# Kernel optimization log

Hardware: AMD Instinct MI355X
Metric: run time of the kernel (lower is better)

The kernel has to match this reference:

```python
import jax, jax.numpy as jnp
import numpy as np
from jax.scipy.special import logsumexp

N_STATES = 512
VOCAB = 10000
BATCH = 64
T_MAX = 1024


def setup_inputs() -> dict:
    key = jax.random.key(0)
    k1, k2, k3, k4, k5 = jax.random.split(key, 5)
    x = jax.random.randint(k1, (BATCH, T_MAX), 0, VOCAB)
    T = jax.random.randint(k2, (BATCH,), 1, T_MAX + 1)  # lengths in [1, T_max]
    priors = jax.random.normal(k3, (N_STATES,), dtype=jnp.float32)
    trans = jax.random.normal(k4, (N_STATES, N_STATES), dtype=jnp.float32)
    emit = jax.random.normal(k5, (N_STATES, VOCAB), dtype=jnp.float32)
    return {"x": x, "T": T, "priors": priors, "trans": trans, "emit": emit}


def reference(x, T, priors, trans, emit):
    # x: (B, Tmax) int, T: (B,) int lengths
    log_pi = jax.nn.log_softmax(priors)            # (N,)
    log_T = jax.nn.log_softmax(trans, axis=0)      # (N, N), columns normalized (dim=0 in torch)
    log_E = jax.nn.log_softmax(emit, axis=1)       # (N, M)

    em = log_E.T[x]                                # (B, Tmax, N) emission log-probs per timestep
    la0 = em[:, 0] + log_pi                        # (B, N)

    def step(la_prev, em_t):
        # out[b, j] = logsumexp_k log_T[j, k] + la_prev[b, k]
        la_new = em_t + logsumexp(log_T[None, :, :] + la_prev[:, None, :], axis=2)
        return la_new, logsumexp(la_new, axis=1)   # carry, per-step log-sum over states

    _, sums = jax.lax.scan(step, la0, jnp.moveaxis(em[:, 1:], 1, 0))  # sums: (Tmax-1, B)
    log_sums = jnp.concatenate([logsumexp(la0, axis=1)[None, :], sums], axis=0)  # (Tmax, B)

    idx = jnp.clip(T, 1, x.shape[1]) - 1           # (B,)
    log_probs = jnp.take_along_axis(log_sums.T, idx[:, None], axis=1)  # (B, 1)
    return log_probs
```

## Files before the change

kernel.cpp:

```cpp
#include <hip/hip_runtime.h>
#include <hip/hip_bf16.h>


typedef unsigned long long u64;
typedef unsigned int u32;
typedef unsigned short u16;
using f32x4 = __attribute__((ext_vector_type(4))) float;
using i32x8 = __attribute__((ext_vector_type(8))) int;

#define N_ST 512
#define VOCAB 10000
#define BATCH 64
#define T_MAX 1024

#define WS_EB       0
#define WS_GB       10240000
#define WS_A8       20480000
#define WS_ROWLSE   20742144
#define WS_COLLSE   20744192
#define WS_PINORM   20746240

static __device__ __forceinline__ float bf16f(u16 h) {
    return __uint_as_float((u32)h << 16);
}
static __device__ __forceinline__ u16 bf16enc(float f) {
    u32 u = __float_as_uint(f);
    return (u16)((u + 0x7fffu + ((u >> 16) & 1u)) >> 16);
}

static __device__ __forceinline__ float dec8(u32 b) {
    float nrm = __uint_as_float((b << 20) + 0x3C000000u);
    float dnm = (float)b * 0x1p-9f;
    return b >= 8u ? nrm : dnm;
}

static __device__ __forceinline__ u32 enc_e4m3(float f) {
    if (!(f > 0.f)) return 0u;
    unsigned u = __float_as_uint(f);
    int e = (int)((u >> 23) & 0xff) - 127;
    unsigned m = u & 0x7fffffu;
    if (e > 8 || (e == 8 && m >= 0x700000u)) return 0x7eu;
    if (e >= -6) {
        unsigned mant = m >> 20;
        unsigned rest = m & 0xfffffu;
        if (rest > 0x80000u || (rest == 0x80000u && (mant & 1u))) mant++;
        unsigned r = ((unsigned)(e + 7) << 3) + mant;
        return r > 0x7eu ? 0x7eu : r;
    }
    if (e < -10) return 0u;
    unsigned full = 0x800000u | m;
    int shift = 23 - (e + 9);
    unsigned r = full >> shift;
    unsigned rem = full & ((1u << shift) - 1u);
    unsigned half = 1u << (shift - 1);
    if (rem > half || (rem == half && (r & 1u))) r++;
    return r;
}

template <bool HI>
static __device__ __forceinline__ u32 cvtpk2(float a, float b, u32 old) {
#if __has_builtin(__builtin_amdgcn_cvt_pk_fp8_f32)
    return (u32)__builtin_amdgcn_cvt_pk_fp8_f32(a, b, (int)old, HI);
#else
    unsigned v = enc_e4m3(a) | (enc_e4m3(b) << 8);
    return HI ? ((old & 0x0000ffffu) | (v << 16)) : ((old & 0xffff0000u) | v);
#endif
}

__global__ __launch_bounds__(256) void k_row_lse(const float* __restrict__ emit,
                                                 float* __restrict__ rowLSE) {
    const int n = blockIdx.x;
    const float* row = emit + (size_t)n * VOCAB;
    __shared__ float redm[4], reds[4];
    const int tid = threadIdx.x, lane = tid & 63, wid = tid >> 6;

    float m = -INFINITY;
    for (int i = tid; i < VOCAB; i += 256) m = fmaxf(m, row[i]);
    #pragma unroll
    for (int o = 32; o; o >>= 1) m = fmaxf(m, __shfl_down(m, o));
    if (lane == 0) redm[wid] = m;
    __syncthreads();
    if (tid == 0) redm[0] = fmaxf(fmaxf(redm[0], redm[1]), fmaxf(redm[2], redm[3]));
    __syncthreads();
    m = redm[0];

    float s = 0.f;
    for (int i = tid; i < VOCAB; i += 256) s += __expf(row[i] - m);
    #pragma unroll
    for (int o = 32; o; o >>= 1) s += __shfl_down(s, o);
    if (lane == 0) reds[wid] = s;
    __syncthreads();
    if (tid == 0) rowLSE[n] = m + __logf(reds[0] + reds[1] + reds[2] + reds[3]);
}

__global__ __launch_bounds__(256) void k_expEmitT(const float* __restrict__ emit,
                                                  const float* __restrict__ rowLSE,
                                                  u16* __restrict__ Eb) {
    const size_t gid = (size_t)blockIdx.x * 256 + threadIdx.x;
    const int m = (int)(gid >> 9);
    const int n = (int)(gid & 511);
    Eb[gid] = bf16enc(__expf(emit[(size_t)n * VOCAB + m] - rowLSE[n]));
}

__global__ __launch_bounds__(256) void k_col_lse(const float* __restrict__ trans,
                                                 float* __restrict__ colLSE) {
    const int k = blockIdx.x;
    const int tid = threadIdx.x, lane = tid & 63, wid = tid >> 6;
    __shared__ float redm[4], reds[4];

    float a = trans[(size_t)tid * N_ST + k];
    float b = trans[(size_t)(tid + 256) * N_ST + k];
    float m = fmaxf(a, b);
    #pragma unroll
    for (int o = 32; o; o >>= 1) m = fmaxf(m, __shfl_down(m, o));
    if (lane == 0) redm[wid] = m;
    __syncthreads();
    if (tid == 0) redm[0] = fmaxf(fmaxf(redm[0], redm[1]), fmaxf(redm[2], redm[3]));
    __syncthreads();
    m = redm[0];

    float s = __expf(a - m) + __expf(b - m);
    #pragma unroll
    for (int o = 32; o; o >>= 1) s += __shfl_down(s, o);
    if (lane == 0) reds[wid] = s;
    __syncthreads();
    if (tid == 0) colLSE[k] = m + __logf(reds[0] + reds[1] + reds[2] + reds[3]);
}

__global__ __launch_bounds__(64) void k_packA_fp8(const float* __restrict__ trans,
                                                  const float* __restrict__ colLSE,
                                                  u32* __restrict__ A8) {
    const int f = blockIdx.x;
    const int l = threadIdx.x;
    const int w = f >> 4, ks = (f >> 2) & 3, jt = f & 3;
    const int j = w * 64 + jt * 16 + (l & 15);
    const int k0 = ks * 128 + (l >> 4) * 32;
    u32 dw[8];
    #pragma unroll
    for (int d = 0; d < 8; ++d) {
        float a0 = 256.0f * __expf(trans[(size_t)j * N_ST + k0 + 4 * d + 0] - colLSE[k0 + 4 * d + 0]);
        float a1 = 256.0f * __expf(trans[(size_t)j * N_ST + k0 + 4 * d + 1] - colLSE[k0 + 4 * d + 1]);
        float a2 = 256.0f * __expf(trans[(size_t)j * N_ST + k0 + 4 * d + 2] - colLSE[k0 + 4 * d + 2]);
        float a3 = 256.0f * __expf(trans[(size_t)j * N_ST + k0 + 4 * d + 3] - colLSE[k0 + 4 * d + 3]);
        u32 pk = cvtpk2<false>(a0, a1, 0u);
        dw[d] = cvtpk2<true>(a2, a3, pk);
    }
    u32* dst = A8 + (size_t)f * 512 + l * 8;
    *(uint4*)dst       = make_uint4(dw[0], dw[1], dw[2], dw[3]);
    *(uint4*)(dst + 4) = make_uint4(dw[4], dw[5], dw[6], dw[7]);
}

__global__ __launch_bounds__(512) void k_pinorm(const float* __restrict__ priors,
                                                float* __restrict__ pinorm) {
    const int j = threadIdx.x, lane = j & 63, wid = j >> 6;
    __shared__ float redm[8], reds[8];
    float v = priors[j];

    float m = v;
    #pragma unroll
    for (int o = 32; o; o >>= 1) m = fmaxf(m, __shfl_down(m, o));
    if (lane == 0) redm[wid] = m;
    __syncthreads();
    if (j == 0) {
        float r = redm[0];
        for (int i = 1; i < 8; ++i) r = fmaxf(r, redm[i]);
        redm[0] = r;
    }
    __syncthreads();
    m = redm[0];

    float s = __expf(v - m);
    #pragma unroll
    for (int o = 32; o; o >>= 1) s += __shfl_down(s, o);
    if (lane == 0) reds[wid] = s;
    __syncthreads();
    if (j == 0) {
        float r = 0.f;
        for (int i = 0; i < 8; ++i) r += reds[i];
        reds[0] = r;
    }
    __syncthreads();
    pinorm[j] = __expf(v - m) / reds[0];
}

__global__ __launch_bounds__(256) void k_G(const u16* __restrict__ Eb,
                                           const float* __restrict__ trans,
                                           const float* __restrict__ colLSE,
                                           u16* __restrict__ Gb) {
    __shared__ float Es[16][512];
    const int m0 = blockIdx.x * 16;
    const int tid = threadIdx.x;
    for (int idx = tid; idx < 16 * 512; idx += 256)
        Es[idx >> 9][idx & 511] = bf16f(Eb[(size_t)(m0 + (idx >> 9)) * 512 + (idx & 511)]);
    __syncthreads();

    const int k0 = tid, k1 = tid + 256;
    const float c0 = colLSE[k0], c1 = colLSE[k1];
    float acc0[16], acc1[16];
    #pragma unroll
    for (int mi = 0; mi < 16; ++mi) { acc0[mi] = 0.f; acc1[mi] = 0.f; }

    for (int j = 0; j < 512; ++j) {
        float a0 = __expf(trans[(size_t)j * N_ST + k0] - c0);
        float a1 = __expf(trans[(size_t)j * N_ST + k1] - c1);
        #pragma unroll
        for (int mi = 0; mi < 16; ++mi) {
            float e = Es[mi][j];
            acc0[mi] = fmaf(e, a0, acc0[mi]);
            acc1[mi] = fmaf(e, a1, acc1[mi]);
        }
    }
    #pragma unroll
    for (int mi = 0; mi < 16; ++mi) {
        Gb[(size_t)(m0 + mi) * N_ST + k0] = bf16enc(acc0[mi]);
        Gb[(size_t)(m0 + mi) * N_ST + k1] = bf16enc(acc1[mi]);
    }
}

#define UNIT_SCALES 0x7f7f7f7f

#define STEP_BODY(EU, GU, EP, GP)                                               \
  {                                                                             \
    const int xpre = xnext;                                                     \
    GP = *(const uint4*)((const char*)Gb + ((size_t)xpre << 10) + (l << 4));    \
    _Pragma("unroll")                                                           \
    for (int jt = 0; jt < 4; ++jt)                                              \
      EP[jt] = *(const u64*)(Eb + (size_t)xpre * N_ST + wbase + jt * 16 + rbase); \
    xnext = xb[(t + 2 <= Tf) ? (t + 2) : Tf];                                   \
    const u64 vown = vq[p][l];                                                  \
    const u32* vbase = (const u32*)&vq[p][0];                                   \
    f32x4 ac0={0,0,0,0}, ac1={0,0,0,0}, ac2={0,0,0,0}, ac3={0,0,0,0};           \
    _Pragma("unroll")                                                           \
    for (int ks = 0; ks < 4; ++ks) {                                            \
      const uint4 b0 = *(const uint4*)(vbase + ks * 32 + grp * 8);              \
      const uint4 b1 = *(const uint4*)(vbase + ks * 32 + grp * 8 + 4);          \
      const i32x8 bq = {(int)b0.x, (int)b0.y, (int)b0.z, (int)b0.w,             \
                        (int)b1.x, (int)b1.y, (int)b1.z, (int)b1.w};            \
      ac0 = __builtin_amdgcn_mfma_scale_f32_16x16x128_f8f6f4(                   \
                af[ks * 4 + 0], bq, ac0, 0, 0, 0, UNIT_SCALES, 0, UNIT_SCALES); \
      ac1 = __builtin_amdgcn_mfma_scale_f32_16x16x128_f8f6f4(                   \
                af[ks * 4 + 1], bq, ac1, 0, 0, 0, UNIT_SCALES, 0, UNIT_SCALES); \
      ac2 = __builtin_amdgcn_mfma_scale_f32_16x16x128_f8f6f4(                   \
                af[ks * 4 + 2], bq, ac2, 0, 0, 0, UNIT_SCALES, 0, UNIT_SCALES); \
      ac3 = __builtin_amdgcn_mfma_scale_f32_16x16x128_f8f6f4(                   \
                af[ks * 4 + 3], bq, ac3, 0, 0, 0, UNIT_SCALES, 0, UNIT_SCALES); \
    }                                                                           \
    float gv = 0.f;                                                             \
    {                                                                           \
      const u32 gw[4] = {GU.x, GU.y, GU.z, GU.w};                               \
      _Pragma("unroll")                                                         \
      for (int i = 0; i < 4; ++i) {                                             \
        float g0 = bf16f((u16)(gw[i] & 0xffffu));                               \
        float g1 = bf16f((u16)(gw[i] >> 16));                                   \
        float v0 = dec8((u32)(vown >> (16 * i)) & 0xffu);                       \
        float v1 = dec8((u32)(vown >> (16 * i + 8)) & 0xffu);                   \
        gv = fmaf(g0, v0, gv);                                                  \
        gv = fmaf(g1, v1, gv);                                                  \
      }                                                                         \
      _Pragma("unroll")                                                         \
      for (int o = 1; o <= 32; o <<= 1) gv += __shfl_xor(gv, o);                \
    }                                                                           \
    float wv2[16];                                                              \
    _Pragma("unroll")                                                           \
    for (int r = 0; r < 4; ++r) {                                               \
      wv2[0 + r]  = bf16f((u16)(EU[0] >> (16 * r))) * ac0[r];                   \
      wv2[4 + r]  = bf16f((u16)(EU[1] >> (16 * r))) * ac1[r];                   \
      wv2[8 + r]  = bf16f((u16)(EU[2] >> (16 * r))) * ac2[r];                   \
      wv2[12 + r] = bf16f((u16)(EU[3] >> (16 * r))) * ac3[r];                   \
    }                                                                           \
    if (t == Tf) {                                                              \
      float s2 = 0.f;                                                           \
      _Pragma("unroll")                                                         \
      for (int i = 0; i < 16; ++i) s2 += wv2[i];                                \
      s2 += __shfl_xor(s2, 16);                                                 \
      s2 += __shfl_xor(s2, 32);                                                 \
      if (l == 0) red[wid] = s2;                                                \
      __syncthreads();                                                          \
      const float Se = red[0] + red[1] + red[2] + red[3] +                      \
                       red[4] + red[5] + red[6] + red[7];                       \
      if (tid == 0) out[b] = L + __logf(Se) - (float)Tb * LN256;                \
    } else {                                                                    \
      L += __logf(gv);                                                          \
      const float sc = 1.0f / gv;                                               \
      if ((l & 15) == 0) {                                                      \
        u32* vw = (u32*)&vq[p ^ 1][0];                                          \
        _Pragma("unroll")                                                       \
        for (int jt = 0; jt < 4; ++jt) {                                        \
          u32 pk = cvtpk2<false>(wv2[jt * 4 + 0] * sc, wv2[jt * 4 + 1] * sc, 0u); \
          pk = cvtpk2<true>(wv2[jt * 4 + 2] * sc, wv2[jt * 4 + 3] * sc, pk);    \
          vw[(wbase >> 2) + jt * 4 + grp] = pk;                                 \
        }                                                                       \
      }                                                                         \
      __syncthreads();                                                          \
      p ^= 1;                                                                   \
    }                                                                           \
  }

__global__ __launch_bounds__(512, 2) void hmm_main(const int* __restrict__ x,
                                                   const int* __restrict__ T,
                                                   const u16* __restrict__ Eb,
                                                   const u32* __restrict__ A8,
                                                   const u16* __restrict__ Gb,
                                                   const float* __restrict__ pinorm,
                                                   float* __restrict__ out) {
    __shared__ u64 vq[2][64];
    __shared__ float red[8];
    const int b = blockIdx.x;
    const int tid = threadIdx.x;
    const int l = tid & 63;
    const int wid = tid >> 6;
    const int grp = l >> 4;
    const int wbase = wid * 64;
    const int rbase = grp * 4;
    const float LN256 = 5.545177444479562f;

    int Tb = T[b];
    Tb = Tb < 1 ? 1 : (Tb > T_MAX ? T_MAX : Tb);
    const int* xb = x + (size_t)b * T_MAX;

    i32x8 af[16];
    {
        const u32* ap = A8 + (size_t)wid * 16 * 512 + l * 8;
        #pragma unroll
        for (int i = 0; i < 16; ++i) {
            uint4 lo = *(const uint4*)(ap + (size_t)i * 512);
            uint4 hi = *(const uint4*)(ap + (size_t)i * 512 + 4);
            af[i] = i32x8{(int)lo.x, (int)lo.y, (int)lo.z, (int)lo.w,
                          (int)hi.x, (int)hi.y, (int)hi.z, (int)hi.w};
        }
    }

    const int x0 = xb[0];
    const int x1 = xb[1];
    u64 eA[4], eB[4];
    uint4 gA, gB;
    gA = *(const uint4*)((const char*)Gb + ((size_t)x1 << 10) + (l << 4));
    #pragma unroll
    for (int jt = 0; jt < 4; ++jt)
        eA[jt] = *(const u64*)(Eb + (size_t)x1 * N_ST + wbase + jt * 16 + rbase);

    float wv[16];
    float s = 0.f;
    #pragma unroll
    for (int jt = 0; jt < 4; ++jt) {
        u64 eraw = *(const u64*)(Eb + (size_t)x0 * N_ST + wbase + jt * 16 + rbase);
        #pragma unroll
        for (int r = 0; r < 4; ++r) {
            const int j = wbase + jt * 16 + rbase + r;
            float e = bf16f((u16)(eraw >> (16 * r)));
            float t0 = e * pinorm[j];
            wv[jt * 4 + r] = t0;
            s += t0;
        }
    }
    s += __shfl_xor(s, 16);
    s += __shfl_xor(s, 32);
    if (l == 0) red[wid] = s;
    __syncthreads();
    float S0 = red[0] + red[1] + red[2] + red[3] + red[4] + red[5] + red[6] + red[7];
    float L = __logf(S0);
    if (Tb == 1) {
        if (tid == 0) out[b] = L;
        return;
    }
    __syncthreads();
    {
        const float sc = 256.0f / S0;
        if ((l & 15) == 0) {
            u32* vw = (u32*)&vq[0][0];
            #pragma unroll
            for (int jt = 0; jt < 4; ++jt) {
                u32 pk = cvtpk2<false>(wv[jt * 4 + 0] * sc, wv[jt * 4 + 1] * sc, 0u);
                pk = cvtpk2<true>(wv[jt * 4 + 2] * sc, wv[jt * 4 + 3] * sc, pk);
                vw[(wbase >> 2) + jt * 4 + grp] = pk;
            }
        }
    }
    __syncthreads();

    const int Tf = Tb - 1;
    int p = 0;
    int xnext = xb[(2 <= Tf) ? 2 : Tf];
    for (int t = 1;;) {
        STEP_BODY(eA, gA, eB, gB)
        if (t == Tf) break;
        ++t;
        STEP_BODY(eB, gB, eA, gA)
        if (t == Tf) break;
        ++t;
    }
}

extern "C" void kernel_launch(void* const* d_in, const int* in_sizes, int n_in,
                              void* d_out, int out_size, void* d_ws, size_t ws_size,
                              hipStream_t stream) {
    const int*   x      = (const int*)d_in[0];
    const int*   T      = (const int*)d_in[1];
    const float* priors = (const float*)d_in[2];
    const float* trans  = (const float*)d_in[3];
    const float* emit   = (const float*)d_in[4];
    float* out = (float*)d_out;

    char* ws = (char*)d_ws;
    u16*   Eb     = (u16*)(ws + WS_EB);
    u16*   Gb     = (u16*)(ws + WS_GB);
    u32*   A8     = (u32*)(ws + WS_A8);
    float* rowLSE = (float*)(ws + WS_ROWLSE);
    float* colLSE = (float*)(ws + WS_COLLSE);
    float* pinorm = (float*)(ws + WS_PINORM);

    k_row_lse<<<N_ST, 256, 0, stream>>>(emit, rowLSE);
    k_expEmitT<<<(VOCAB * N_ST) / 256, 256, 0, stream>>>(emit, rowLSE, Eb);
    k_col_lse<<<N_ST, 256, 0, stream>>>(trans, colLSE);
    k_packA_fp8<<<128, 64, 0, stream>>>(trans, colLSE, A8);
    k_pinorm<<<1, 512, 0, stream>>>(priors, pinorm);
    k_G<<<VOCAB / 16, 256, 0, stream>>>(Eb, trans, colLSE, Gb);

    hmm_main<<<BATCH, 512, 0, stream>>>(x, T, Eb, A8, Gb, pinorm, out);
}
```

Measured before the change: 1.332 ms.

## Quantize transition matrix to block-scaled FP4 with per-row E8M0 scales

Replaces the FP8 packing of the exponentiated transition matrix with FP4 (E2M1) values plus a per-32-element E8M0 block scale, and feeds them to the scaled MFMA with the A operand format set to FP4 and the scale selected per opsel. This halves the register footprint of the resident A fragments (16 x uint4 instead of 16 x i32x8), which could ease register pressure and raise occupancy, and may reduce MFMA cost. The price is a much coarser quantization of transition probabilities, which risks accuracy loss, and the scale packing and indexing are intricate.

```diff
diff --git a/kernel.cpp b/kernel.cpp
--- a/kernel.cpp
+++ b/kernel.cpp
@@ -15,10 +15,11 @@
 
 #define WS_EB       0
 #define WS_GB       10240000
-#define WS_A8       20480000
-#define WS_ROWLSE   20742144
-#define WS_COLLSE   20744192
-#define WS_PINORM   20746240
+#define WS_A4       20480000
+#define WS_ASC      20611072
+#define WS_ROWLSE   20643840
+#define WS_COLLSE   20645888
+#define WS_PINORM   20647936
 
 static __device__ __forceinline__ float bf16f(u16 h) {
     return __uint_as_float((u32)h << 16);
@@ -127,27 +128,38 @@
     if (tid == 0) colLSE[k] = m + __logf(reds[0] + reds[1] + reds[2] + reds[3]);
 }
 
-__global__ __launch_bounds__(64) void k_packA_fp8(const float* __restrict__ trans,
+__global__ __launch_bounds__(64) void k_packA_fp4(const float* __restrict__ trans,
                                                   const float* __restrict__ colLSE,
-                                                  u32* __restrict__ A8) {
+                                                  u32* __restrict__ A4,
+                                                  unsigned char* __restrict__ ASC) {
     const int f = blockIdx.x;
     const int l = threadIdx.x;
     const int w = f >> 4, ks = (f >> 2) & 3, jt = f & 3;
     const int j = w * 64 + jt * 16 + (l & 15);
     const int k0 = ks * 128 + (l >> 4) * 32;
-    u32 dw[8];
-    #pragma unroll
-    for (int d = 0; d < 8; ++d) {
-        float a0 = 256.0f * __expf(trans[(size_t)j * N_ST + k0 + 4 * d + 0] - colLSE[k0 + 4 * d + 0]);
-        float a1 = 256.0f * __expf(trans[(size_t)j * N_ST + k0 + 4 * d + 1] - colLSE[k0 + 4 * d + 1]);
-        float a2 = 256.0f * __expf(trans[(size_t)j * N_ST + k0 + 4 * d + 2] - colLSE[k0 + 4 * d + 2]);
-        float a3 = 256.0f * __expf(trans[(size_t)j * N_ST + k0 + 4 * d + 3] - colLSE[k0 + 4 * d + 3]);
-        u32 pk = cvtpk2<false>(a0, a1, 0u);
-        dw[d] = cvtpk2<true>(a2, a3, pk);
-    }
-    u32* dst = A8 + (size_t)f * 512 + l * 8;
-    *(uint4*)dst       = make_uint4(dw[0], dw[1], dw[2], dw[3]);
-    *(uint4*)(dst + 4) = make_uint4(dw[4], dw[5], dw[6], dw[7]);
+
+    float e[32];
+    float m = 0.f;
+    #pragma unroll
+    for (int k = 0; k < 32; ++k) {
+        e[k] = 256.0f * __expf(trans[(size_t)j * N_ST + k0 + k] - colLSE[k0 + k]);
+        m = fmaxf(m, e[k]);
+    }
+    const int eexp = (int)ceilf(log2f(m * (1.0f / 6.0f)));
+    const float inv = exp2f((float)(-eexp));
+
+    u32 dw[4] = {0u, 0u, 0u, 0u};
+    #pragma unroll
+    for (int k = 0; k < 32; ++k) {
+        const float xv = e[k] * inv;
+        u32 q = xv < 0.25f ? 0u : xv < 0.75f ? 1u : xv < 1.25f ? 2u :
+                xv < 1.75f ? 3u : xv < 2.5f  ? 4u : xv < 3.5f  ? 5u :
+                xv < 5.0f  ? 6u : 7u;
+        dw[k >> 3] |= q << (4 * (k & 7));
+    }
+    u32* dst = A4 + (size_t)f * 256 + l * 4;
+    *(uint4*)dst = make_uint4(dw[0], dw[1], dw[2], dw[3]);
+    ASC[(size_t)(((w * 4 + ks) * 64 + l) * 4) + jt] = (unsigned char)(127 + eexp);
 }
 
 __global__ __launch_bounds__(512) void k_pinorm(const float* __restrict__ priors,
@@ -218,6 +230,7 @@
 }
 
 #define UNIT_SCALES 0x7f7f7f7f
+#define AFRAG(i) (i32x8{(int)af[i].x, (int)af[i].y, (int)af[i].z, (int)af[i].w, 0, 0, 0, 0})
 
 #define STEP_BODY(EU, GU, EP, GP)                                               \
   {                                                                             \
@@ -237,13 +250,13 @@
       const i32x8 bq = {(int)b0.x, (int)b0.y, (int)b0.z, (int)b0.w,             \
                         (int)b1.x, (int)b1.y, (int)b1.z, (int)b1.w};            \
       ac0 = __builtin_amdgcn_mfma_scale_f32_16x16x128_f8f6f4(                   \
-                af[ks * 4 + 0], bq, ac0, 0, 0, 0, UNIT_SCALES, 0, UNIT_SCALES); \
+                AFRAG(ks * 4 + 0), bq, ac0, 4, 0, 0, (int)asc[ks], 0, UNIT_SCALES); \
       ac1 = __builtin_amdgcn_mfma_scale_f32_16x16x128_f8f6f4(                   \
-                af[ks * 4 + 1], bq, ac1, 0, 0, 0, UNIT_SCALES, 0, UNIT_SCALES); \
+                AFRAG(ks * 4 + 1), bq, ac1, 4, 0, 1, (int)asc[ks], 0, UNIT_SCALES); \
       ac2 = __builtin_amdgcn_mfma_scale_f32_16x16x128_f8f6f4(                   \
-                af[ks * 4 + 2], bq, ac2, 0, 0, 0, UNIT_SCALES, 0, UNIT_SCALES); \
+                AFRAG(ks * 4 + 2), bq, ac2, 4, 0, 2, (int)asc[ks], 0, UNIT_SCALES); \
       ac3 = __builtin_amdgcn_mfma_scale_f32_16x16x128_f8f6f4(                   \
-                af[ks * 4 + 3], bq, ac3, 0, 0, 0, UNIT_SCALES, 0, UNIT_SCALES); \
+                AFRAG(ks * 4 + 3), bq, ac3, 4, 0, 3, (int)asc[ks], 0, UNIT_SCALES); \
     }                                                                           \
     float gv = 0.f;                                                             \
     {                                                                           \
@@ -299,7 +312,8 @@
 __global__ __launch_bounds__(512, 2) void hmm_main(const int* __restrict__ x,
                                                    const int* __restrict__ T,
                                                    const u16* __restrict__ Eb,
-                                                   const u32* __restrict__ A8,
+                                                   const u32* __restrict__ A4,
+                                                   const u32* __restrict__ ASC,
                                                    const u16* __restrict__ Gb,
                                                    const float* __restrict__ pinorm,
                                                    float* __restrict__ out) {
@@ -318,16 +332,16 @@
     Tb = Tb < 1 ? 1 : (Tb > T_MAX ? T_MAX : Tb);
     const int* xb = x + (size_t)b * T_MAX;
 
-    i32x8 af[16];
+    uint4 af[16];
+    u32 asc[4];
     {
-        const u32* ap = A8 + (size_t)wid * 16 * 512 + l * 8;
+        const u32* ap = A4 + (size_t)wid * 16 * 256 + l * 4;
         #pragma unroll
-        for (int i = 0; i < 16; ++i) {
-            uint4 lo = *(const uint4*)(ap + (size_t)i * 512);
-            uint4 hi = *(const uint4*)(ap + (size_t)i * 512 + 4);
-            af[i] = i32x8{(int)lo.x, (int)lo.y, (int)lo.z, (int)lo.w,
-                          (int)hi.x, (int)hi.y, (int)hi.z, (int)hi.w};
-        }
+        for (int i = 0; i < 16; ++i)
+            af[i] = *(const uint4*)(ap + (size_t)i * 256);
+        #pragma unroll
+        for (int d = 0; d < 4; ++d)
+            asc[d] = ASC[(wid * 4 + d) * 64 + l];
     }
 
     const int x0 = xb[0];
@@ -404,7 +418,8 @@
     char* ws = (char*)d_ws;
     u16*   Eb     = (u16*)(ws + WS_EB);
     u16*   Gb     = (u16*)(ws + WS_GB);
-    u32*   A8     = (u32*)(ws + WS_A8);
+    u32*   A4     = (u32*)(ws + WS_A4);
+    unsigned char* ASCb = (unsigned char*)(ws + WS_ASC);
     float* rowLSE = (float*)(ws + WS_ROWLSE);
     float* colLSE = (float*)(ws + WS_COLLSE);
     float* pinorm = (float*)(ws + WS_PINORM);
@@ -412,9 +427,9 @@
     k_row_lse<<<N_ST, 256, 0, stream>>>(emit, rowLSE);
     k_expEmitT<<<(VOCAB * N_ST) / 256, 256, 0, stream>>>(emit, rowLSE, Eb);
     k_col_lse<<<N_ST, 256, 0, stream>>>(trans, colLSE);
-    k_packA_fp8<<<128, 64, 0, stream>>>(trans, colLSE, A8);
+    k_packA_fp4<<<128, 64, 0, stream>>>(trans, colLSE, A4, ASCb);
     k_pinorm<<<1, 512, 0, stream>>>(priors, pinorm);
     k_G<<<VOCAB / 16, 256, 0, stream>>>(Eb, trans, colLSE, Gb);
 
-    hmm_main<<<BATCH, 512, 0, stream>>>(x, T, Eb, A8, Gb, pinorm, out);
-}
+    hmm_main<<<BATCH, 512, 0, stream>>>(x, T, Eb, A4, (const u32*)ASCb, Gb, pinorm, out);
+}
```

Result: slower. 1.383 ms (+3.8%).
